# Optimization experiments

Hardware: AMD Instinct MI355X
Metric: run time of the kernel (lower is better)

The kernel has to match this reference:

```python
import jax, jax.numpy as jnp
import numpy as np

N_PATIENT = 50000
N_GENE = 20000
N_EDGE = 640000
P_DIM, G_DIM, H, OUT = 64, 32, 128, 8


def setup_inputs() -> dict:
    key = jax.random.key(0)
    ks = jax.random.split(key, 20)
    s = 0.02
    return {
        "x_patient": jax.random.normal(ks[0], (N_PATIENT, P_DIM), jnp.float32),
        "x_gene": jax.random.normal(ks[1], (N_GENE, G_DIM), jnp.float32),
        "edge_index": jax.random.randint(ks[2], (2, N_EDGE), 0, N_GENE, jnp.int32),
        # patient MLP
        "W_p1": jax.random.normal(ks[3], (P_DIM, H), jnp.float32) * s,
        "b_p1": jnp.zeros((H,), jnp.float32),
        "W_p2": jax.random.normal(ks[4], (H, H), jnp.float32) * s,
        "b_p2": jnp.zeros((H,), jnp.float32),
        # gene MLP
        "W_g1": jax.random.normal(ks[5], (G_DIM, H), jnp.float32) * s,
        "b_g1": jnp.zeros((H,), jnp.float32),
        "W_g2": jax.random.normal(ks[6], (H, H), jnp.float32) * s,
        "b_g2": jnp.zeros((H,), jnp.float32),
        # SAGEConv 1: lin_l acts on aggregated src, lin_r (root) on dst
        "W1_l": jax.random.normal(ks[7], (H, H), jnp.float32) * s,
        "b1_l": jnp.zeros((H,), jnp.float32),
        "W1_r": jax.random.normal(ks[8], (H, H), jnp.float32) * s,
        # SAGEConv 2
        "W2_l": jax.random.normal(ks[9], (H, H), jnp.float32) * s,
        "b2_l": jnp.zeros((H,), jnp.float32),
        "W2_r": jax.random.normal(ks[10], (H, H), jnp.float32) * s,
        # final fc
        "W_fc": jax.random.normal(ks[11], (H, OUT), jnp.float32) * s,
        "b_fc": jnp.zeros((OUT,), jnp.float32),
    }


def reference(x_patient, x_gene, edge_index,
              W_p1, b_p1, W_p2, b_p2,
              W_g1, b_g1, W_g2, b_g2,
              W1_l, b1_l, W1_r,
              W2_l, b2_l, W2_r,
              W_fc, b_fc):
    # node-type MLPs
    p = jax.nn.relu(x_patient @ W_p1 + b_p1) @ W_p2 + b_p2   # [N_P, H]
    g = jax.nn.relu(x_gene @ W_g1 + b_g1) @ W_g2 + b_g2       # [N_G, H]

    src, dst = edge_index[0], edge_index[1]
    # gene_x is unchanged between layers, so the sum-aggregate is identical
    # for both SAGEConv layers: compute the gather + segment-sum once.
    agg = jax.ops.segment_sum(g[src], dst, num_segments=x_patient.shape[0])  # [N_P, H]

    # SAGEConv(aggr='sum'): out = lin_l(agg) + lin_r(x_dst), bias in lin_l
    p = jax.nn.relu(agg @ W1_l + b1_l + p @ W1_r)
    p = jax.nn.relu(agg @ W2_l + b2_l + p @ W2_r)
    return p @ W_fc + b_fc  # [N_P, OUT]
```

## Files before the change

### kernel.cpp

```cpp
#include <hip/hip_runtime.h>

#define NP 50000
#define NG 20000
#define NE 640000
#define PD 64
#define GD 32
#define HD 128
#define OD 8
#define CAP 96
#define FILLB 125
#define EPB 5120

using f32x4 = __attribute__((ext_vector_type(4))) float;
using s16x8 = __attribute__((ext_vector_type(8))) short;

__device__ __forceinline__ unsigned short f2bf(float f) {
    union { float f; unsigned u; } v; v.f = f;
    const unsigned r = v.u + 0x7FFFu + ((v.u >> 16) & 1u);
    return (unsigned short)(r >> 16);
}
__device__ __forceinline__ float bfpair_lo(unsigned v) {
    union { unsigned u; float f; } x; x.u = v << 16; return x.f;
}
__device__ __forceinline__ float bfpair_hi(unsigned v) {
    union { unsigned u; float f; } x; x.u = v & 0xFFFF0000u; return x.f;
}

#define TOT_SWZ 112640

__global__ __launch_bounds__(256) void swz_kernel(
    const float* __restrict__ Wp1, const float* __restrict__ Wp2,
    const float* __restrict__ W1l, const float* __restrict__ W1r,
    const float* __restrict__ W2l, const float* __restrict__ W2r,
    const float* __restrict__ Wfc,
    const float* __restrict__ Wg1, const float* __restrict__ Wg2,
    unsigned short* __restrict__ wswz)
{
    const int u = blockIdx.x * 256 + threadIdx.x;
    if (u < TOT_SWZ) {
        const float* src; int K, Nr, doff;
        if      (u <   8192) { src = Wp1; K =  64; Nr = HD; doff = 0; }
        else if (u <  24576) { src = Wp2; K = 128; Nr = HD; doff = 8192; }
        else if (u <  40960) { src = W1l; K = 128; Nr = HD; doff = 24576; }
        else if (u <  57344) { src = W1r; K = 128; Nr = HD; doff = 40960; }
        else if (u <  73728) { src = W2l; K = 128; Nr = HD; doff = 57344; }
        else if (u <  90112) { src = W2r; K = 128; Nr = HD; doff = 73728; }
        else if (u <  92160) { src = Wfc; K = 128; Nr = OD; doff = 90112; }
        else if (u <  96256) { src = Wg1; K =  32; Nr = HD; doff = 92160; }
        else                 { src = Wg2; K = 128; Nr = HD; doff = 96256; }
        const int e  = u - doff;
        const int j  = e & 7;
        const int ln = (e >> 3) & 63;
        const int f  = e >> 9;
        const int KC = K >> 5;
        const int c  = f % KC;
        const int n0 = f / KC;
        const int k  = c * 32 + (ln >> 4) * 8 + j;
        const int n  = n0 * 16 + (ln & 15);
        wswz[u] = f2bf((n < Nr) ? src[k * Nr + n] : 0.f);
    }
}

#define GENE_TILES 313

__global__ __launch_bounds__(256) void genefill_kernel(
    const float* __restrict__ xg,
    const unsigned short* __restrict__ wswz,
    const float* __restrict__ bg1, const float* __restrict__ bg2,
    unsigned short* __restrict__ g,
    const int* __restrict__ ei, int* __restrict__ hist)
{
    __shared__ __align__(16) char smem[NG * 4];
    if (blockIdx.x >= GENE_TILES) {
        int* cnt = (int*)smem;
        const int tid = threadIdx.x;
#pragma unroll
        for (int k = 0; k < 20; ++k) {
            const int idx = k * 256 + tid;
            if (idx < NG / 4) ((int4*)cnt)[idx] = (int4){0, 0, 0, 0};
        }
        __syncthreads();
        const int base = (blockIdx.x - GENE_TILES) * EPB;
#pragma unroll
        for (int it = 0; it < 5; ++it) {
            const int e0 = base + it * 1024 + tid;
            const int d0 = ei[NE + e0];
            const int d1 = ei[NE + e0 + 256];
            const int d2 = ei[NE + e0 + 512];
            const int d3 = ei[NE + e0 + 768];
            atomicAdd(&cnt[d0], 1);
            atomicAdd(&cnt[d1], 1);
            atomicAdd(&cnt[d2], 1);
            atomicAdd(&cnt[d3], 1);
        }
        __syncthreads();
        int* Hb = hist + (blockIdx.x - GENE_TILES) * NG;
#pragma unroll
        for (int k = 0; k < 20; ++k) {
            const int idx = k * 256 + tid;
            if (idx < NG / 4) ((int4*)Hb)[idx] = ((int4*)cnt)[idx];
        }
        return;
    }
    const unsigned short* wg1 = wswz + 92160;
    const unsigned short* wg2 = wswz + 96256;

    const int lane = threadIdx.x & 63;
    const int wid  = threadIdx.x >> 6;
    const int quad = lane >> 4;
    const int l16  = lane & 15;
    const int row0 = blockIdx.x * 64 + wid * 16;
    const int arow = min(row0 + l16, NG - 1);
    unsigned short* X = (unsigned short*)smem + wid * 16 * 136;
    const f32x4 Z = {0.f, 0.f, 0.f, 0.f};

    s16x8 a;
    {
        const float* xr = xg + (size_t)arow * GD + quad * 8;
        const f32x4 u0 = *(const f32x4*)xr;
        const f32x4 u1 = *(const f32x4*)(xr + 4);
#pragma unroll
        for (int j = 0; j < 4; ++j) {
            a[j]     = (short)f2bf(u0[j]);
            a[4 + j] = (short)f2bf(u1[j]);
        }
    }
    f32x4 C[8];
#pragma unroll
    for (int n = 0; n < 8; ++n) {
        const s16x8 b = *(const s16x8*)&wg1[(n * 64 + lane) * 8];
        C[n] = __builtin_amdgcn_mfma_f32_16x16x32_bf16(a, b, Z, 0, 0, 0);
    }
#pragma unroll
    for (int n = 0; n < 8; ++n) {
        const float bias = bg1[n * 16 + l16];
#pragma unroll
        for (int r = 0; r < 4; ++r)
            X[(quad * 4 + r) * 136 + n * 16 + l16] = f2bf(fmaxf(C[n][r] + bias, 0.f));
    }
    __syncthreads();
    s16x8 pa[4];
#pragma unroll
    for (int c = 0; c < 4; ++c) pa[c] = *(const s16x8*)&X[l16 * 136 + c * 32 + quad * 8];
#pragma unroll
    for (int n = 0; n < 8; ++n) {
        C[n] = Z;
#pragma unroll
        for (int c = 0; c < 4; ++c) {
            const s16x8 b = *(const s16x8*)&wg2[((n * 4 + c) * 64 + lane) * 8];
            C[n] = __builtin_amdgcn_mfma_f32_16x16x32_bf16(pa[c], b, C[n], 0, 0, 0);
        }
    }
#pragma unroll
    for (int n = 0; n < 8; ++n) {
        const float bias = bg2[n * 16 + l16];
#pragma unroll
        for (int r = 0; r < 4; ++r) {
            const int row = row0 + quad * 4 + r;
            if (row < NG) g[(size_t)row * HD + n * 16 + l16] = f2bf(C[n][r] + bias);
        }
    }
}

__global__ __launch_bounds__(256) void scan_kernel(
    int* __restrict__ hist, int* __restrict__ cursor)
{
    const int d = blockIdx.x * 256 + threadIdx.x;
    if (d >= NG) return;
    int run = 0;
#pragma unroll 5
    for (int b = 0; b < FILLB; ++b) {
        const int t = hist[b * NG + d];
        hist[b * NG + d] = run;
        run += t;
    }
    cursor[d] = run;
}

__global__ __launch_bounds__(256) void place_kernel(
    const int* __restrict__ ei, const int* __restrict__ hist,
    unsigned short* __restrict__ pad)
{
    __shared__ __align__(16) int cnt[NG];
    const int tid = threadIdx.x;
    const int* Hb = hist + blockIdx.x * NG;
#pragma unroll
    for (int k = 0; k < 20; ++k) {
        const int idx = k * 256 + tid;
        if (idx < NG / 4) ((int4*)cnt)[idx] = ((const int4*)Hb)[idx];
    }
    __syncthreads();
    const int base = blockIdx.x * EPB;
#pragma unroll
    for (int it = 0; it < 5; ++it) {
        const int e0 = base + it * 1024 + tid;
        const int s0 = ei[e0];       const int d0 = ei[NE + e0];
        const int s1 = ei[e0 + 256]; const int d1 = ei[NE + e0 + 256];
        const int s2 = ei[e0 + 512]; const int d2 = ei[NE + e0 + 512];
        const int s3 = ei[e0 + 768]; const int d3 = ei[NE + e0 + 768];
        { const int p = atomicAdd(&cnt[d0], 1); if (p < CAP) pad[d0 * CAP + p] = (unsigned short)s0; }
        { const int p = atomicAdd(&cnt[d1], 1); if (p < CAP) pad[d1 * CAP + p] = (unsigned short)s1; }
        { const int p = atomicAdd(&cnt[d2], 1); if (p < CAP) pad[d2 * CAP + p] = (unsigned short)s2; }
        { const int p = atomicAdd(&cnt[d3], 1); if (p < CAP) pad[d3 * CAP + p] = (unsigned short)s3; }
    }
}

__global__ __launch_bounds__(256) void agg_kernel(
    const int* __restrict__ cursor, const unsigned short* __restrict__ pad,
    const unsigned short* __restrict__ g, unsigned short* __restrict__ aggb)
{
    const int row  = blockIdx.x * 4 + (threadIdx.x >> 6);
    const int lane = threadIdx.x & 63;
    const int grp  = lane >> 4;
    const int sub  = lane & 15;

    float acc[8] = {0.f, 0.f, 0.f, 0.f, 0.f, 0.f, 0.f, 0.f};
    const int cnt = min(cursor[row], CAP);
    const size_t rb = (size_t)row * CAP;
    for (int i = grp * 4; i < cnt; i += 16) {
        const ushort4 q = *(const ushort4*)&pad[rb + i];
        int r0 = q.x, r1 = q.y, r2 = q.z, r3 = q.w;
        const bool v1 = (i + 1) < cnt, v2 = (i + 2) < cnt, v3 = (i + 3) < cnt;
        r1 = v1 ? r1 : r0;  r2 = v2 ? r2 : r0;  r3 = v3 ? r3 : r0;
        const float s1 = v1 ? 1.f : 0.f, s2 = v2 ? 1.f : 0.f, s3 = v3 ? 1.f : 0.f;
        const s16x8 g0 = *(const s16x8*)&g[(size_t)r0 * HD + sub * 8];
        const s16x8 g1 = *(const s16x8*)&g[(size_t)r1 * HD + sub * 8];
        const s16x8 g2 = *(const s16x8*)&g[(size_t)r2 * HD + sub * 8];
        const s16x8 g3 = *(const s16x8*)&g[(size_t)r3 * HD + sub * 8];
        const unsigned* d0 = (const unsigned*)&g0;
        const unsigned* d1 = (const unsigned*)&g1;
        const unsigned* d2 = (const unsigned*)&g2;
        const unsigned* d3 = (const unsigned*)&g3;
#pragma unroll
        for (int k = 0; k < 4; ++k) {
            acc[2 * k]     += bfpair_lo(d0[k]);
            acc[2 * k + 1] += bfpair_hi(d0[k]);
            acc[2 * k]     = fmaf(bfpair_lo(d1[k]), s1, acc[2 * k]);
            acc[2 * k + 1] = fmaf(bfpair_hi(d1[k]), s1, acc[2 * k + 1]);
            acc[2 * k]     = fmaf(bfpair_lo(d2[k]), s2, acc[2 * k]);
            acc[2 * k + 1] = fmaf(bfpair_hi(d2[k]), s2, acc[2 * k + 1]);
            acc[2 * k]     = fmaf(bfpair_lo(d3[k]), s3, acc[2 * k]);
            acc[2 * k + 1] = fmaf(bfpair_hi(d3[k]), s3, acc[2 * k + 1]);
        }
    }
#pragma unroll
    for (int k = 0; k < 8; ++k) {
        acc[k] += __shfl_xor(acc[k], 16);
        acc[k] += __shfl_xor(acc[k], 32);
    }
    if (lane < 16) {
        unsigned o[4];
#pragma unroll
        for (int k = 0; k < 4; ++k)
            o[k] = (unsigned)f2bf(acc[2 * k]) | ((unsigned)f2bf(acc[2 * k + 1]) << 16);
        *(int4*)&aggb[(size_t)row * HD + lane * 8] = *(int4*)o;
    }
}

__global__ __launch_bounds__(256) void patient_kernel(
    const float* __restrict__ xp, const unsigned short* __restrict__ aggb,
    const unsigned short* __restrict__ wswz,
    const float* __restrict__ bp1, const float* __restrict__ bp2,
    const float* __restrict__ b1l, const float* __restrict__ b2l,
    const float* __restrict__ bfc,
    float* __restrict__ out)
{
    const unsigned short* wp1 = wswz + 0;
    const unsigned short* wp2 = wswz + 8192;
    const unsigned short* w1l = wswz + 24576;
    const unsigned short* w1r = wswz + 40960;
    const unsigned short* w2l = wswz + 57344;
    const unsigned short* w2r = wswz + 73728;
    const unsigned short* wfc = wswz + 90112;

    __shared__ __align__(16) unsigned short XA[128 * 136];
    __shared__ __align__(16) unsigned short AG[128 * 136];

    const int tid  = threadIdx.x;
    const int lane = tid & 63;
    const int wid  = tid >> 6;
    const int quad = lane >> 4;
    const int l16  = lane & 15;
    const int brow = blockIdx.x * 128;
    const bool hasAgg = (brow < NG);
    const int nA = wid * 2, nB = wid * 2 + 1;
    const f32x4 Z = {0.f, 0.f, 0.f, 0.f};

#pragma unroll
    for (int s = 0; s < 8; ++s) {
        const int slot = s * 256 + tid;
        const int r  = slot >> 4;
        const int cv = slot & 15;
        const f32x4 u = *(const f32x4*)&xp[(size_t)min(brow + r, NP - 1) * PD + cv * 4];
        unsigned short o[4];
#pragma unroll
        for (int j = 0; j < 4; ++j) o[j] = f2bf(u[j]);
        *(ushort4*)&XA[r * 136 + cv * 4] = *(ushort4*)o;
    }
    if (hasAgg) {
#pragma unroll
        for (int s = 0; s < 8; ++s) {
            const int slot = s * 256 + tid;
            const int r  = slot >> 4;
            const int cv = slot & 15;
            const int gr = brow + r;
            s16x8 v = {0, 0, 0, 0, 0, 0, 0, 0};
            if (gr < NG) v = *(const s16x8*)&aggb[(size_t)gr * HD + cv * 8];
            *(s16x8*)&AG[r * 136 + cv * 8] = v;
        }
    }
    __syncthreads();

    f32x4 acc[8][2];

#pragma unroll
    for (int rt = 0; rt < 8; ++rt) { acc[rt][0] = Z; acc[rt][1] = Z; }
#pragma unroll
    for (int c = 0; c < 2; ++c) {
        const s16x8 b0 = *(const s16x8*)&wp1[((nA * 2 + c) * 64 + lane) * 8];
        const s16x8 b1 = *(const s16x8*)&wp1[((nB * 2 + c) * 64 + lane) * 8];
#pragma unroll
        for (int rt = 0; rt < 8; ++rt) {
            const s16x8 a = *(const s16x8*)&XA[(rt * 16 + l16) * 136 + c * 32 + quad * 8];
            acc[rt][0] = __builtin_amdgcn_mfma_f32_16x16x32_bf16(a, b0, acc[rt][0], 0, 0, 0);
            acc[rt][1] = __builtin_amdgcn_mfma_f32_16x16x32_bf16(a, b1, acc[rt][1], 0, 0, 0);
        }
    }
    __syncthreads();
#pragma unroll
    for (int t = 0; t < 2; ++t) {
        const int n = wid * 2 + t;
        const float bias = bp1[n * 16 + l16];
#pragma unroll
        for (int rt = 0; rt < 8; ++rt)
#pragma unroll
            for (int r = 0; r < 4; ++r)
                XA[(rt * 16 + quad * 4 + r) * 136 + n * 16 + l16] =
                    f2bf(fmaxf(acc[rt][t][r] + bias, 0.f));
    }
    __syncthreads();

#pragma unroll
    for (int rt = 0; rt < 8; ++rt) { acc[rt][0] = Z; acc[rt][1] = Z; }
#pragma unroll
    for (int c = 0; c < 4; ++c) {
        const s16x8 b0 = *(const s16x8*)&wp2[((nA * 4 + c) * 64 + lane) * 8];
        const s16x8 b1 = *(const s16x8*)&wp2[((nB * 4 + c) * 64 + lane) * 8];
#pragma unroll
        for (int rt = 0; rt < 8; ++rt) {
            const s16x8 a = *(const s16x8*)&XA[(rt * 16 + l16) * 136 + c * 32 + quad * 8];
            acc[rt][0] = __builtin_amdgcn_mfma_f32_16x16x32_bf16(a, b0, acc[rt][0], 0, 0, 0);
            acc[rt][1] = __builtin_amdgcn_mfma_f32_16x16x32_bf16(a, b1, acc[rt][1], 0, 0, 0);
        }
    }
    __syncthreads();
#pragma unroll
    for (int t = 0; t < 2; ++t) {
        const int n = wid * 2 + t;
        const float bias = bp2[n * 16 + l16];
#pragma unroll
        for (int rt = 0; rt < 8; ++rt)
#pragma unroll
            for (int r = 0; r < 4; ++r)
                XA[(rt * 16 + quad * 4 + r) * 136 + n * 16 + l16] =
                    f2bf(acc[rt][t][r] + bias);
    }
    __syncthreads();

#pragma unroll
    for (int rt = 0; rt < 8; ++rt) { acc[rt][0] = Z; acc[rt][1] = Z; }
    if (hasAgg) {
#pragma unroll
        for (int c = 0; c < 4; ++c) {
            const s16x8 br0 = *(const s16x8*)&w1r[((nA * 4 + c) * 64 + lane) * 8];
            const s16x8 br1 = *(const s16x8*)&w1r[((nB * 4 + c) * 64 + lane) * 8];
            const s16x8 bl0 = *(const s16x8*)&w1l[((nA * 4 + c) * 64 + lane) * 8];
            const s16x8 bl1 = *(const s16x8*)&w1l[((nB * 4 + c) * 64 + lane) * 8];
#pragma unroll
            for (int rt = 0; rt < 8; ++rt) {
                const s16x8 ap = *(const s16x8*)&XA[(rt * 16 + l16) * 136 + c * 32 + quad * 8];
                const s16x8 ag = *(const s16x8*)&AG[(rt * 16 + l16) * 136 + c * 32 + quad * 8];
                acc[rt][0] = __builtin_amdgcn_mfma_f32_16x16x32_bf16(ap, br0, acc[rt][0], 0, 0, 0);
                acc[rt][0] = __builtin_amdgcn_mfma_f32_16x16x32_bf16(ag, bl0, acc[rt][0], 0, 0, 0);
                acc[rt][1] = __builtin_amdgcn_mfma_f32_16x16x32_bf16(ap, br1, acc[rt][1], 0, 0, 0);
                acc[rt][1] = __builtin_amdgcn_mfma_f32_16x16x32_bf16(ag, bl1, acc[rt][1], 0, 0, 0);
            }
        }
    } else {
#pragma unroll
        for (int c = 0; c < 4; ++c) {
            const s16x8 br0 = *(const s16x8*)&w1r[((nA * 4 + c) * 64 + lane) * 8];
            const s16x8 br1 = *(const s16x8*)&w1r[((nB * 4 + c) * 64 + lane) * 8];
#pragma unroll
            for (int rt = 0; rt < 8; ++rt) {
                const s16x8 ap = *(const s16x8*)&XA[(rt * 16 + l16) * 136 + c * 32 + quad * 8];
                acc[rt][0] = __builtin_amdgcn_mfma_f32_16x16x32_bf16(ap, br0, acc[rt][0], 0, 0, 0);
                acc[rt][1] = __builtin_amdgcn_mfma_f32_16x16x32_bf16(ap, br1, acc[rt][1], 0, 0, 0);
            }
        }
    }
    __syncthreads();
#pragma unroll
    for (int t = 0; t < 2; ++t) {
        const int n = wid * 2 + t;
        const float bias = b1l[n * 16 + l16];
#pragma unroll
        for (int rt = 0; rt < 8; ++rt)
#pragma unroll
            for (int r = 0; r < 4; ++r)
                XA[(rt * 16 + quad * 4 + r) * 136 + n * 16 + l16] =
                    f2bf(fmaxf(acc[rt][t][r] + bias, 0.f));
    }
    __syncthreads();

#pragma unroll
    for (int rt = 0; rt < 8; ++rt) { acc[rt][0] = Z; acc[rt][1] = Z; }
    if (hasAgg) {
#pragma unroll
        for (int c = 0; c < 4; ++c) {
            const s16x8 br0 = *(const s16x8*)&w2r[((nA * 4 + c) * 64 + lane) * 8];
            const s16x8 br1 = *(const s16x8*)&w2r[((nB * 4 + c) * 64 + lane) * 8];
            const s16x8 bl0 = *(const s16x8*)&w2l[((nA * 4 + c) * 64 + lane) * 8];
            const s16x8 bl1 = *(const s16x8*)&w2l[((nB * 4 + c) * 64 + lane) * 8];
#pragma unroll
            for (int rt = 0; rt < 8; ++rt) {
                const s16x8 ap = *(const s16x8*)&XA[(rt * 16 + l16) * 136 + c * 32 + quad * 8];
                const s16x8 ag = *(const s16x8*)&AG[(rt * 16 + l16) * 136 + c * 32 + quad * 8];
                acc[rt][0] = __builtin_amdgcn_mfma_f32_16x16x32_bf16(ap, br0, acc[rt][0], 0, 0, 0);
                acc[rt][0] = __builtin_amdgcn_mfma_f32_16x16x32_bf16(ag, bl0, acc[rt][0], 0, 0, 0);
                acc[rt][1] = __builtin_amdgcn_mfma_f32_16x16x32_bf16(ap, br1, acc[rt][1], 0, 0, 0);
                acc[rt][1] = __builtin_amdgcn_mfma_f32_16x16x32_bf16(ag, bl1, acc[rt][1], 0, 0, 0);
            }
        }
    } else {
#pragma unroll
        for (int c = 0; c < 4; ++c) {
            const s16x8 br0 = *(const s16x8*)&w2r[((nA * 4 + c) * 64 + lane) * 8];
            const s16x8 br1 = *(const s16x8*)&w2r[((nB * 4 + c) * 64 + lane) * 8];
#pragma unroll
            for (int rt = 0; rt < 8; ++rt) {
                const s16x8 ap = *(const s16x8*)&XA[(rt * 16 + l16) * 136 + c * 32 + quad * 8];
                acc[rt][0] = __builtin_amdgcn_mfma_f32_16x16x32_bf16(ap, br0, acc[rt][0], 0, 0, 0);
                acc[rt][1] = __builtin_amdgcn_mfma_f32_16x16x32_bf16(ap, br1, acc[rt][1], 0, 0, 0);
            }
        }
    }
    __syncthreads();
#pragma unroll
    for (int t = 0; t < 2; ++t) {
        const int n = wid * 2 + t;
        const float bias = b2l[n * 16 + l16];
#pragma unroll
        for (int rt = 0; rt < 8; ++rt)
#pragma unroll
            for (int r = 0; r < 4; ++r)
                XA[(rt * 16 + quad * 4 + r) * 136 + n * 16 + l16] =
                    f2bf(fmaxf(acc[rt][t][r] + bias, 0.f));
    }
    __syncthreads();

    {
        f32x4 co[2] = {Z, Z};
#pragma unroll
        for (int c = 0; c < 4; ++c) {
            const s16x8 b = *(const s16x8*)&wfc[(c * 64 + lane) * 8];
#pragma unroll
            for (int j = 0; j < 2; ++j) {
                const int rt = wid * 2 + j;
                const s16x8 a = *(const s16x8*)&XA[(rt * 16 + l16) * 136 + c * 32 + quad * 8];
                co[j] = __builtin_amdgcn_mfma_f32_16x16x32_bf16(a, b, co[j], 0, 0, 0);
            }
        }
        if (l16 < OD) {
            const float bias = bfc[l16];
#pragma unroll
            for (int j = 0; j < 2; ++j)
#pragma unroll
                for (int r = 0; r < 4; ++r) {
                    const int row = brow + (wid * 2 + j) * 16 + quad * 4 + r;
                    if (row < NP) out[(size_t)row * OD + l16] = co[j][r] + bias;
                }
        }
    }
}

extern "C" void kernel_launch(void* const* d_in, const int* in_sizes, int n_in,
                              void* d_out, int out_size, void* d_ws, size_t ws_size,
                              hipStream_t stream)
{
    const float* xp  = (const float*)d_in[0];
    const float* xg  = (const float*)d_in[1];
    const int*   ei  = (const int*)d_in[2];
    const float* Wp1 = (const float*)d_in[3];
    const float* bp1 = (const float*)d_in[4];
    const float* Wp2 = (const float*)d_in[5];
    const float* bp2 = (const float*)d_in[6];
    const float* Wg1 = (const float*)d_in[7];
    const float* bg1 = (const float*)d_in[8];
    const float* Wg2 = (const float*)d_in[9];
    const float* bg2 = (const float*)d_in[10];
    const float* W1l = (const float*)d_in[11];
    const float* b1l = (const float*)d_in[12];
    const float* W1r = (const float*)d_in[13];
    const float* W2l = (const float*)d_in[14];
    const float* b2l = (const float*)d_in[15];
    const float* W2r = (const float*)d_in[16];
    const float* Wfc = (const float*)d_in[17];
    const float* bfc = (const float*)d_in[18];
    float* out = (float*)d_out;

    char* ws = (char*)d_ws;
    unsigned short* g_b   = (unsigned short*)(ws + 0);
    unsigned short* wswz  = (unsigned short*)(ws + 5120000);
    int*            cursor= (int*)(ws + 5345280);
    int*            hist  = (int*)(ws + 5425280);
    unsigned short* pad   = (unsigned short*)(ws + 15425280);
    unsigned short* agg_b = (unsigned short*)(ws + 19265280);

    swz_kernel<<<(TOT_SWZ + 255) / 256, 256, 0, stream>>>(
        Wp1, Wp2, W1l, W1r, W2l, W2r, Wfc, Wg1, Wg2, wswz);

    genefill_kernel<<<GENE_TILES + FILLB, 256, 0, stream>>>(
        xg, wswz, bg1, bg2, g_b, ei, hist);

    scan_kernel<<<(NG + 255) / 256, 256, 0, stream>>>(hist, cursor);

    place_kernel<<<FILLB, 256, 0, stream>>>(ei, hist, pad);

    agg_kernel<<<NG / 4, 256, 0, stream>>>(cursor, pad, g_b, agg_b);

    patient_kernel<<<(NP + 127) / 128, 256, 0, stream>>>(
        xp, agg_b, wswz, bp1, bp2, b1l, b2l, bfc, out);
}
```

Before: 163.1 us.

## Replace histogram/scan edge bucketing with global atomics and restructure kernel schedule

Drops the per-block histogram, scan and shared-memory place kernels. Edges are now bucketed directly with global atomicAdd on a cursor array that the swizzle kernel zeroes, and this placement runs in the same launch as the gene MLP. The aggregation blocks are merged into the patient-MLP launch so the gather overlaps with the patient rows that have no aggregate. Patient rows below NG write their MLP output to a buffer, and a separate SAGE kernel finishes them. The gains are fewer launches and less hist traffic; the costs are contention on global atomics and an extra round trip through memory for p.

Result: slower. 194.1 us (+19.0%).

```diff
diff --git a/kernel.cpp b/kernel.cpp
--- a/kernel.cpp
+++ b/kernel.cpp
@@ -8,8 +8,10 @@
 #define HD 128
 #define OD 8
 #define CAP 96
-#define FILLB 125
-#define EPB 5120
+#define PLACEB 625
+#define GENE_TILES 313
+#define PATB 391
+#define SAGEB 157
 
 using f32x4 = __attribute__((ext_vector_type(4))) float;
 using s16x8 = __attribute__((ext_vector_type(8))) short;
@@ -34,7 +36,7 @@
     const float* __restrict__ W2l, const float* __restrict__ W2r,
     const float* __restrict__ Wfc,
     const float* __restrict__ Wg1, const float* __restrict__ Wg2,
-    unsigned short* __restrict__ wswz)
+    unsigned short* __restrict__ wswz, int* __restrict__ cursor)
 {
     const int u = blockIdx.x * 256 + threadIdx.x;
     if (u < TOT_SWZ) {
@@ -58,48 +60,32 @@
         const int k  = c * 32 + (ln >> 4) * 8 + j;
         const int n  = n0 * 16 + (ln & 15);
         wswz[u] = f2bf((n < Nr) ? src[k * Nr + n] : 0.f);
-    }
-}
-
-#define GENE_TILES 313
-
-__global__ __launch_bounds__(256) void genefill_kernel(
+    } else {
+        const int d = u - TOT_SWZ;
+        if (d < NG) cursor[d] = 0;
+    }
+}
+
+__global__ __launch_bounds__(256) void geneplace_kernel(
     const float* __restrict__ xg,
     const unsigned short* __restrict__ wswz,
     const float* __restrict__ bg1, const float* __restrict__ bg2,
     unsigned short* __restrict__ g,
-    const int* __restrict__ ei, int* __restrict__ hist)
+    const int* __restrict__ ei,
+    int* __restrict__ cursor, unsigned short* __restrict__ pad)
 {
-    __shared__ __align__(16) char smem[NG * 4];
+    __shared__ __align__(16) unsigned short smem[4 * 16 * 136];
     if (blockIdx.x >= GENE_TILES) {
-        int* cnt = (int*)smem;
-        const int tid = threadIdx.x;
-#pragma unroll
-        for (int k = 0; k < 20; ++k) {
-            const int idx = k * 256 + tid;
-            if (idx < NG / 4) ((int4*)cnt)[idx] = (int4){0, 0, 0, 0};
-        }
-        __syncthreads();
-        const int base = (blockIdx.x - GENE_TILES) * EPB;
-#pragma unroll
-        for (int it = 0; it < 5; ++it) {
-            const int e0 = base + it * 1024 + tid;
-            const int d0 = ei[NE + e0];
-            const int d1 = ei[NE + e0 + 256];
-            const int d2 = ei[NE + e0 + 512];
-            const int d3 = ei[NE + e0 + 768];
-            atomicAdd(&cnt[d0], 1);
-            atomicAdd(&cnt[d1], 1);
-            atomicAdd(&cnt[d2], 1);
-            atomicAdd(&cnt[d3], 1);
-        }
-        __syncthreads();
-        int* Hb = hist + (blockIdx.x - GENE_TILES) * NG;
-#pragma unroll
-        for (int k = 0; k < 20; ++k) {
-            const int idx = k * 256 + tid;
-            if (idx < NG / 4) ((int4*)Hb)[idx] = ((int4*)cnt)[idx];
-        }
+        const int base = (blockIdx.x - GENE_TILES) * 1024;
+        const int e0 = base + threadIdx.x;
+        const int s0 = ei[e0];       const int d0 = ei[NE + e0];
+        const int s1 = ei[e0 + 256]; const int d1 = ei[NE + e0 + 256];
+        const int s2 = ei[e0 + 512]; const int d2 = ei[NE + e0 + 512];
+        const int s3 = ei[e0 + 768]; const int d3 = ei[NE + e0 + 768];
+        { const int p = atomicAdd(&cursor[d0], 1); if (p < CAP) pad[d0 * CAP + p] = (unsigned short)s0; }
+        { const int p = atomicAdd(&cursor[d1], 1); if (p < CAP) pad[d1 * CAP + p] = (unsigned short)s1; }
+        { const int p = atomicAdd(&cursor[d2], 1); if (p < CAP) pad[d2 * CAP + p] = (unsigned short)s2; }
+        { const int p = atomicAdd(&cursor[d3], 1); if (p < CAP) pad[d3 * CAP + p] = (unsigned short)s3; }
         return;
     }
     const unsigned short* wg1 = wswz + 92160;
@@ -111,7 +97,7 @@
     const int l16  = lane & 15;
     const int row0 = blockIdx.x * 64 + wid * 16;
     const int arow = min(row0 + l16, NG - 1);
-    unsigned short* X = (unsigned short*)smem + wid * 16 * 136;
+    unsigned short* X = smem + wid * 16 * 136;
     const f32x4 Z = {0.f, 0.f, 0.f, 0.f};
 
     s16x8 a;
@@ -162,119 +148,74 @@
     }
 }
 
-__global__ __launch_bounds__(256) void scan_kernel(
-    int* __restrict__ hist, int* __restrict__ cursor)
-{
-    const int d = blockIdx.x * 256 + threadIdx.x;
-    if (d >= NG) return;
-    int run = 0;
-#pragma unroll 5
-    for (int b = 0; b < FILLB; ++b) {
-        const int t = hist[b * NG + d];
-        hist[b * NG + d] = run;
-        run += t;
-    }
-    cursor[d] = run;
-}
-
-__global__ __launch_bounds__(256) void place_kernel(
-    const int* __restrict__ ei, const int* __restrict__ hist,
-    unsigned short* __restrict__ pad)
-{
-    __shared__ __align__(16) int cnt[NG];
-    const int tid = threadIdx.x;
-    const int* Hb = hist + blockIdx.x * NG;
-#pragma unroll
-    for (int k = 0; k < 20; ++k) {
-        const int idx = k * 256 + tid;
-        if (idx < NG / 4) ((int4*)cnt)[idx] = ((const int4*)Hb)[idx];
-    }
-    __syncthreads();
-    const int base = blockIdx.x * EPB;
-#pragma unroll
-    for (int it = 0; it < 5; ++it) {
-        const int e0 = base + it * 1024 + tid;
-        const int s0 = ei[e0];       const int d0 = ei[NE + e0];
-        const int s1 = ei[e0 + 256]; const int d1 = ei[NE + e0 + 256];
-        const int s2 = ei[e0 + 512]; const int d2 = ei[NE + e0 + 512];
-        const int s3 = ei[e0 + 768]; const int d3 = ei[NE + e0 + 768];
-        { const int p = atomicAdd(&cnt[d0], 1); if (p < CAP) pad[d0 * CAP + p] = (unsigned short)s0; }
-        { const int p = atomicAdd(&cnt[d1], 1); if (p < CAP) pad[d1 * CAP + p] = (unsigned short)s1; }
-        { const int p = atomicAdd(&cnt[d2], 1); if (p < CAP) pad[d2 * CAP + p] = (unsigned short)s2; }
-        { const int p = atomicAdd(&cnt[d3], 1); if (p < CAP) pad[d3 * CAP + p] = (unsigned short)s3; }
-    }
-}
-
-__global__ __launch_bounds__(256) void agg_kernel(
+__global__ __launch_bounds__(256) void patient3_kernel(
+    const float* __restrict__ xp,
+    const unsigned short* __restrict__ g,
     const int* __restrict__ cursor, const unsigned short* __restrict__ pad,
-    const unsigned short* __restrict__ g, unsigned short* __restrict__ aggb)
-{
-    const int row  = blockIdx.x * 4 + (threadIdx.x >> 6);
-    const int lane = threadIdx.x & 63;
-    const int grp  = lane >> 4;
-    const int sub  = lane & 15;
-
-    float acc[8] = {0.f, 0.f, 0.f, 0.f, 0.f, 0.f, 0.f, 0.f};
-    const int cnt = min(cursor[row], CAP);
-    const size_t rb = (size_t)row * CAP;
-    for (int i = grp * 4; i < cnt; i += 16) {
-        const ushort4 q = *(const ushort4*)&pad[rb + i];
-        int r0 = q.x, r1 = q.y, r2 = q.z, r3 = q.w;
-        const bool v1 = (i + 1) < cnt, v2 = (i + 2) < cnt, v3 = (i + 3) < cnt;
-        r1 = v1 ? r1 : r0;  r2 = v2 ? r2 : r0;  r3 = v3 ? r3 : r0;
-        const float s1 = v1 ? 1.f : 0.f, s2 = v2 ? 1.f : 0.f, s3 = v3 ? 1.f : 0.f;
-        const s16x8 g0 = *(const s16x8*)&g[(size_t)r0 * HD + sub * 8];
-        const s16x8 g1 = *(const s16x8*)&g[(size_t)r1 * HD + sub * 8];
-        const s16x8 g2 = *(const s16x8*)&g[(size_t)r2 * HD + sub * 8];
-        const s16x8 g3 = *(const s16x8*)&g[(size_t)r3 * HD + sub * 8];
-        const unsigned* d0 = (const unsigned*)&g0;
-        const unsigned* d1 = (const unsigned*)&g1;
-        const unsigned* d2 = (const unsigned*)&g2;
-        const unsigned* d3 = (const unsigned*)&g3;
-#pragma unroll
-        for (int k = 0; k < 4; ++k) {
-            acc[2 * k]     += bfpair_lo(d0[k]);
-            acc[2 * k + 1] += bfpair_hi(d0[k]);
-            acc[2 * k]     = fmaf(bfpair_lo(d1[k]), s1, acc[2 * k]);
-            acc[2 * k + 1] = fmaf(bfpair_hi(d1[k]), s1, acc[2 * k + 1]);
-            acc[2 * k]     = fmaf(bfpair_lo(d2[k]), s2, acc[2 * k]);
-            acc[2 * k + 1] = fmaf(bfpair_hi(d2[k]), s2, acc[2 * k + 1]);
-            acc[2 * k]     = fmaf(bfpair_lo(d3[k]), s3, acc[2 * k]);
-            acc[2 * k + 1] = fmaf(bfpair_hi(d3[k]), s3, acc[2 * k + 1]);
-        }
-    }
-#pragma unroll
-    for (int k = 0; k < 8; ++k) {
-        acc[k] += __shfl_xor(acc[k], 16);
-        acc[k] += __shfl_xor(acc[k], 32);
-    }
-    if (lane < 16) {
-        unsigned o[4];
-#pragma unroll
-        for (int k = 0; k < 4; ++k)
-            o[k] = (unsigned)f2bf(acc[2 * k]) | ((unsigned)f2bf(acc[2 * k + 1]) << 16);
-        *(int4*)&aggb[(size_t)row * HD + lane * 8] = *(int4*)o;
-    }
-}
-
-__global__ __launch_bounds__(256) void patient_kernel(
-    const float* __restrict__ xp, const unsigned short* __restrict__ aggb,
     const unsigned short* __restrict__ wswz,
     const float* __restrict__ bp1, const float* __restrict__ bp2,
     const float* __restrict__ b1l, const float* __restrict__ b2l,
     const float* __restrict__ bfc,
+    unsigned short* __restrict__ p_b, unsigned short* __restrict__ aggb,
     float* __restrict__ out)
 {
+    __shared__ __align__(16) unsigned short XA[128 * 136];
+
+    if (blockIdx.x >= PATB) {
+        const int row  = (blockIdx.x - PATB) * 4 + (threadIdx.x >> 6);
+        const int lane = threadIdx.x & 63;
+        const int grp  = lane >> 4;
+        const int sub  = lane & 15;
+
+        float acc[8] = {0.f, 0.f, 0.f, 0.f, 0.f, 0.f, 0.f, 0.f};
+        const int cnt = min(cursor[row], CAP);
+        const size_t rb = (size_t)row * CAP;
+        for (int i = grp * 4; i < cnt; i += 16) {
+            const ushort4 q = *(const ushort4*)&pad[rb + i];
+            int r0 = q.x, r1 = q.y, r2 = q.z, r3 = q.w;
+            const bool v1 = (i + 1) < cnt, v2 = (i + 2) < cnt, v3 = (i + 3) < cnt;
+            r1 = v1 ? r1 : r0;  r2 = v2 ? r2 : r0;  r3 = v3 ? r3 : r0;
+            const float s1 = v1 ? 1.f : 0.f, s2 = v2 ? 1.f : 0.f, s3 = v3 ? 1.f : 0.f;
+            const s16x8 g0 = *(const s16x8*)&g[(size_t)r0 * HD + sub * 8];
+            const s16x8 g1 = *(const s16x8*)&g[(size_t)r1 * HD + sub * 8];
+            const s16x8 g2 = *(const s16x8*)&g[(size_t)r2 * HD + sub * 8];
+            const s16x8 g3 = *(const s16x8*)&g[(size_t)r3 * HD + sub * 8];
+            const unsigned* d0 = (const unsigned*)&g0;
+            const unsigned* d1 = (const unsigned*)&g1;
+            const unsigned* d2 = (const unsigned*)&g2;
+            const unsigned* d3 = (const unsigned*)&g3;
+#pragma unroll
+            for (int k = 0; k < 4; ++k) {
+                acc[2 * k]     += bfpair_lo(d0[k]);
+                acc[2 * k + 1] += bfpair_hi(d0[k]);
+                acc[2 * k]     = fmaf(bfpair_lo(d1[k]), s1, acc[2 * k]);
+                acc[2 * k + 1] = fmaf(bfpair_hi(d1[k]), s1, acc[2 * k + 1]);
+                acc[2 * k]     = fmaf(bfpair_lo(d2[k]), s2, acc[2 * k]);
+                acc[2 * k + 1] = fmaf(bfpair_hi(d2[k]), s2, acc[2 * k + 1]);
+                acc[2 * k]     = fmaf(bfpair_lo(d3[k]), s3, acc[2 * k]);
+                acc[2 * k + 1] = fmaf(bfpair_hi(d3[k]), s3, acc[2 * k + 1]);
+            }
+        }
+#pragma unroll
+        for (int k = 0; k < 8; ++k) {
+            acc[k] += __shfl_xor(acc[k], 16);
+            acc[k] += __shfl_xor(acc[k], 32);
+        }
+        if (lane < 16) {
+            unsigned o[4];
+#pragma unroll
+            for (int k = 0; k < 4; ++k)
+                o[k] = (unsigned)f2bf(acc[2 * k]) | ((unsigned)f2bf(acc[2 * k + 1]) << 16);
+            *(int4*)&aggb[(size_t)row * HD + lane * 8] = *(int4*)o;
+        }
+        return;
+    }
+
     const unsigned short* wp1 = wswz + 0;
     const unsigned short* wp2 = wswz + 8192;
-    const unsigned short* w1l = wswz + 24576;
     const unsigned short* w1r = wswz + 40960;
-    const unsigned short* w2l = wswz + 57344;
     const unsigned short* w2r = wswz + 73728;
     const unsigned short* wfc = wswz + 90112;
-
-    __shared__ __align__(16) unsigned short XA[128 * 136];
-    __shared__ __align__(16) unsigned short AG[128 * 136];
 
     const int tid  = threadIdx.x;
     const int lane = tid & 63;
@@ -282,7 +223,6 @@
     const int quad = lane >> 4;
     const int l16  = lane & 15;
     const int brow = blockIdx.x * 128;
-    const bool hasAgg = (brow < NG);
     const int nA = wid * 2, nB = wid * 2 + 1;
     const f32x4 Z = {0.f, 0.f, 0.f, 0.f};
 
@@ -297,18 +237,6 @@
         for (int j = 0; j < 4; ++j) o[j] = f2bf(u[j]);
         *(ushort4*)&XA[r * 136 + cv * 4] = *(ushort4*)o;
     }
-    if (hasAgg) {
-#pragma unroll
-        for (int s = 0; s < 8; ++s) {
-            const int slot = s * 256 + tid;
-            const int r  = slot >> 4;
-            const int cv = slot & 15;
-            const int gr = brow + r;
-            s16x8 v = {0, 0, 0, 0, 0, 0, 0, 0};
-            if (gr < NG) v = *(const s16x8*)&aggb[(size_t)gr * HD + cv * 8];
-            *(s16x8*)&AG[r * 136 + cv * 8] = v;
-        }
-    }
     __syncthreads();
 
     f32x4 acc[8][2];
@@ -353,6 +281,22 @@
             acc[rt][1] = __builtin_amdgcn_mfma_f32_16x16x32_bf16(a, b1, acc[rt][1], 0, 0, 0);
         }
     }
+
+    if (brow < NG) {
+#pragma unroll
+        for (int t = 0; t < 2; ++t) {
+            const int n = wid * 2 + t;
+            const float bias = bp2[n * 16 + l16];
+#pragma unroll
+            for (int rt = 0; rt < 8; ++rt)
+#pragma unroll
+                for (int r = 0; r < 4; ++r)
+                    p_b[(size_t)(brow + rt * 16 + quad * 4 + r) * HD + n * 16 + l16] =
+                        f2bf(acc[rt][t][r] + bias);
+        }
+        return;
+    }
+
     __syncthreads();
 #pragma unroll
     for (int t = 0; t < 2; ++t) {
@@ -369,34 +313,15 @@
 
 #pragma unroll
     for (int rt = 0; rt < 8; ++rt) { acc[rt][0] = Z; acc[rt][1] = Z; }
-    if (hasAgg) {
-#pragma unroll
-        for (int c = 0; c < 4; ++c) {
-            const s16x8 br0 = *(const s16x8*)&w1r[((nA * 4 + c) * 64 + lane) * 8];
-            const s16x8 br1 = *(const s16x8*)&w1r[((nB * 4 + c) * 64 + lane) * 8];
-            const s16x8 bl0 = *(const s16x8*)&w1l[((nA * 4 + c) * 64 + lane) * 8];
-            const s16x8 bl1 = *(const s16x8*)&w1l[((nB * 4 + c) * 64 + lane) * 8];
-#pragma unroll
-            for (int rt = 0; rt < 8; ++rt) {
-                const s16x8 ap = *(const s16x8*)&XA[(rt * 16 + l16) * 136 + c * 32 + quad * 8];
-                const s16x8 ag = *(const s16x8*)&AG[(rt * 16 + l16) * 136 + c * 32 + quad * 8];
-                acc[rt][0] = __builtin_amdgcn_mfma_f32_16x16x32_bf16(ap, br0, acc[rt][0], 0, 0, 0);
-                acc[rt][0] = __builtin_amdgcn_mfma_f32_16x16x32_bf16(ag, bl0, acc[rt][0], 0, 0, 0);
-                acc[rt][1] = __builtin_amdgcn_mfma_f32_16x16x32_bf16(ap, br1, acc[rt][1], 0, 0, 0);
-                acc[rt][1] = __builtin_amdgcn_mfma_f32_16x16x32_bf16(ag, bl1, acc[rt][1], 0, 0, 0);
-            }
-        }
-    } else {
-#pragma unroll
-        for (int c = 0; c < 4; ++c) {
-            const s16x8 br0 = *(const s16x8*)&w1r[((nA * 4 + c) * 64 + lane) * 8];
-            const s16x8 br1 = *(const s16x8*)&w1r[((nB * 4 + c) * 64 + lane) * 8];
-#pragma unroll
-            for (int rt = 0; rt < 8; ++rt) {
-                const s16x8 ap = *(const s16x8*)&XA[(rt * 16 + l16) * 136 + c * 32 + quad * 8];
-                acc[rt][0] = __builtin_amdgcn_mfma_f32_16x16x32_bf16(ap, br0, acc[rt][0], 0, 0, 0);
-                acc[rt][1] = __builtin_amdgcn_mfma_f32_16x16x32_bf16(ap, br1, acc[rt][1], 0, 0, 0);
-            }
+#pragma unroll
+    for (int c = 0; c < 4; ++c) {
+        const s16x8 b0 = *(const s16x8*)&w1r[((nA * 4 + c) * 64 + lane) * 8];
+        const s16x8 b1 = *(const s16x8*)&w1r[((nB * 4 + c) * 64 + lane) * 8];
+#pragma unroll
+        for (int rt = 0; rt < 8; ++rt) {
+            const s16x8 a = *(const s16x8*)&XA[(rt * 16 + l16) * 136 + c * 32 + quad * 8];
+            acc[rt][0] = __builtin_amdgcn_mfma_f32_16x16x32_bf16(a, b0, acc[rt][0], 0, 0, 0);
+            acc[rt][1] = __builtin_amdgcn_mfma_f32_16x16x32_bf16(a, b1, acc[rt][1], 0, 0, 0);
         }
     }
     __syncthreads();
@@ -415,34 +340,144 @@
 
 #pragma unroll
     for (int rt = 0; rt < 8; ++rt) { acc[rt][0] = Z; acc[rt][1] = Z; }
-    if (hasAgg) {
+#pragma unroll
+    for (int c = 0; c < 4; ++c) {
+        const s16x8 b0 = *(const s16x8*)&w2r[((nA * 4 + c) * 64 + lane) * 8];
+        const s16x8 b1 = *(const s16x8*)&w2r[((nB * 4 + c) * 64 + lane) * 8];
+#pragma unroll
+        for (int rt = 0; rt < 8; ++rt) {
+            const s16x8 a = *(const s16x8*)&XA[(rt * 16 + l16) * 136 + c * 32 + quad * 8];
+            acc[rt][0] = __builtin_amdgcn_mfma_f32_16x16x32_bf16(a, b0, acc[rt][0], 0, 0, 0);
+            acc[rt][1] = __builtin_amdgcn_mfma_f32_16x16x32_bf16(a, b1, acc[rt][1], 0, 0, 0);
+        }
+    }
+    __syncthreads();
+#pragma unroll
+    for (int t = 0; t < 2; ++t) {
+        const int n = wid * 2 + t;
+        const float bias = b2l[n * 16 + l16];
+#pragma unroll
+        for (int rt = 0; rt < 8; ++rt)
+#pragma unroll
+            for (int r = 0; r < 4; ++r)
+                XA[(rt * 16 + quad * 4 + r) * 136 + n * 16 + l16] =
+                    f2bf(fmaxf(acc[rt][t][r] + bias, 0.f));
+    }
+    __syncthreads();
+
+    {
+        f32x4 co[2] = {Z, Z};
 #pragma unroll
         for (int c = 0; c < 4; ++c) {
-            const s16x8 br0 = *(const s16x8*)&w2r[((nA * 4 + c) * 64 + lane) * 8];
-            const s16x8 br1 = *(const s16x8*)&w2r[((nB * 4 + c) * 64 + lane) * 8];
-            const s16x8 bl0 = *(const s16x8*)&w2l[((nA * 4 + c) * 64 + lane) * 8];
-            const s16x8 bl1 = *(const s16x8*)&w2l[((nB * 4 + c) * 64 + lane) * 8];
-#pragma unroll
-            for (int rt = 0; rt < 8; ++rt) {
-                const s16x8 ap = *(const s16x8*)&XA[(rt * 16 + l16) * 136 + c * 32 + quad * 8];
-                const s16x8 ag = *(const s16x8*)&AG[(rt * 16 + l16) * 136 + c * 32 + quad * 8];
-                acc[rt][0] = __builtin_amdgcn_mfma_f32_16x16x32_bf16(ap, br0, acc[rt][0], 0, 0, 0);
-                acc[rt][0] = __builtin_amdgcn_mfma_f32_16x16x32_bf16(ag, bl0, acc[rt][0], 0, 0, 0);
-                acc[rt][1] = __builtin_amdgcn_mfma_f32_16x16x32_bf16(ap, br1, acc[rt][1], 0, 0, 0);
-                acc[rt][1] = __builtin_amdgcn_mfma_f32_16x16x32_bf16(ag, bl1, acc[rt][1], 0, 0, 0);
+            const s16x8 b = *(const s16x8*)&wfc[(c * 64 + lane) * 8];
+#pragma unroll
+            for (int j = 0; j < 2; ++j) {
+                const int rt = wid * 2 + j;
+                const s16x8 a = *(const s16x8*)&XA[(rt * 16 + l16) * 136 + c * 32 + quad * 8];
+                co[j] = __builtin_amdgcn_mfma_f32_16x16x32_bf16(a, b, co[j], 0, 0, 0);
             }
         }
-    } else {
-#pragma unroll
-        for (int c = 0; c < 4; ++c) {
-            const s16x8 br0 = *(const s16x8*)&w2r[((nA * 4 + c) * 64 + lane) * 8];
-            const s16x8 br1 = *(const s16x8*)&w2r[((nB * 4 + c) * 64 + lane) * 8];
-#pragma unroll
-            for (int rt = 0; rt < 8; ++rt) {
-                const s16x8 ap = *(const s16x8*)&XA[(rt * 16 + l16) * 136 + c * 32 + quad * 8];
-                acc[rt][0] = __builtin_amdgcn_mfma_f32_16x16x32_bf16(ap, br0, acc[rt][0], 0, 0, 0);
-                acc[rt][1] = __builtin_amdgcn_mfma_f32_16x16x32_bf16(ap, br1, acc[rt][1], 0, 0, 0);
-            }
+        if (l16 < OD) {
+            const float bias = bfc[l16];
+#pragma unroll
+            for (int j = 0; j < 2; ++j)
+#pragma unroll
+                for (int r = 0; r < 4; ++r) {
+                    const int row = brow + (wid * 2 + j) * 16 + quad * 4 + r;
+                    if (row < NP) out[(size_t)row * OD + l16] = co[j][r] + bias;
+                }
+        }
+    }
+}
+
+__global__ __launch_bounds__(256) void sage_kernel(
+    const unsigned short* __restrict__ p_b, const unsigned short* __restrict__ aggb,
+    const unsigned short* __restrict__ wswz,
+    const float* __restrict__ b1l, const float* __restrict__ b2l,
+    const float* __restrict__ bfc,
+    float* __restrict__ out)
+{
+    const unsigned short* w1l = wswz + 24576;
+    const unsigned short* w1r = wswz + 40960;
+    const unsigned short* w2l = wswz + 57344;
+    const unsigned short* w2r = wswz + 73728;
+    const unsigned short* wfc = wswz + 90112;
+
+    __shared__ __align__(16) unsigned short XA[128 * 136];
+    __shared__ __align__(16) unsigned short AG[128 * 136];
+
+    const int tid  = threadIdx.x;
+    const int lane = tid & 63;
+    const int wid  = tid >> 6;
+    const int quad = lane >> 4;
+    const int l16  = lane & 15;
+    const int brow = blockIdx.x * 128;
+    const int nA = wid * 2, nB = wid * 2 + 1;
+    const f32x4 Z = {0.f, 0.f, 0.f, 0.f};
+
+#pragma unroll
+    for (int s = 0; s < 8; ++s) {
+        const int slot = s * 256 + tid;
+        const int r  = slot >> 4;
+        const int cv = slot & 15;
+        const int gr = brow + r;
+        *(s16x8*)&XA[r * 136 + cv * 8] = *(const s16x8*)&p_b[(size_t)gr * HD + cv * 8];
+        s16x8 v = {0, 0, 0, 0, 0, 0, 0, 0};
+        if (gr < NG) v = *(const s16x8*)&aggb[(size_t)gr * HD + cv * 8];
+        *(s16x8*)&AG[r * 136 + cv * 8] = v;
+    }
+    __syncthreads();
+
+    f32x4 acc[8][2];
+
+#pragma unroll
+    for (int rt = 0; rt < 8; ++rt) { acc[rt][0] = Z; acc[rt][1] = Z; }
+#pragma unroll
+    for (int c = 0; c < 4; ++c) {
+        const s16x8 br0 = *(const s16x8*)&w1r[((nA * 4 + c) * 64 + lane) * 8];
+        const s16x8 br1 = *(const s16x8*)&w1r[((nB * 4 + c) * 64 + lane) * 8];
+        const s16x8 bl0 = *(const s16x8*)&w1l[((nA * 4 + c) * 64 + lane) * 8];
+        const s16x8 bl1 = *(const s16x8*)&w1l[((nB * 4 + c) * 64 + lane) * 8];
+#pragma unroll
+        for (int rt = 0; rt < 8; ++rt) {
+            const s16x8 ap = *(const s16x8*)&XA[(rt * 16 + l16) * 136 + c * 32 + quad * 8];
+            const s16x8 ag = *(const s16x8*)&AG[(rt * 16 + l16) * 136 + c * 32 + quad * 8];
+            acc[rt][0] = __builtin_amdgcn_mfma_f32_16x16x32_bf16(ap, br0, acc[rt][0], 0, 0, 0);
+            acc[rt][0] = __builtin_amdgcn_mfma_f32_16x16x32_bf16(ag, bl0, acc[rt][0], 0, 0, 0);
+            acc[rt][1] = __builtin_amdgcn_mfma_f32_16x16x32_bf16(ap, br1, acc[rt][1], 0, 0, 0);
+            acc[rt][1] = __builtin_amdgcn_mfma_f32_16x16x32_bf16(ag, bl1, acc[rt][1], 0, 0, 0);
+        }
+    }
+    __syncthreads();
+#pragma unroll
+    for (int t = 0; t < 2; ++t) {
+        const int n = wid * 2 + t;
+        const float bias = b1l[n * 16 + l16];
+#pragma unroll
+        for (int rt = 0; rt < 8; ++rt)
+#pragma unroll
+            for (int r = 0; r < 4; ++r)
+                XA[(rt * 16 + quad * 4 + r) * 136 + n * 16 + l16] =
+                    f2bf(fmaxf(acc[rt][t][r] + bias, 0.f));
+    }
+    __syncthreads();
+
+#pragma unroll
+    for (int rt = 0; rt < 8; ++rt) { acc[rt][0] = Z; acc[rt][1] = Z; }
+#pragma unroll
+    for (int c = 0; c < 4; ++c) {
+        const s16x8 br0 = *(const s16x8*)&w2r[((nA * 4 + c) * 64 + lane) * 8];
+        const s16x8 br1 = *(const s16x8*)&w2r[((nB * 4 + c) * 64 + lane) * 8];
+        const s16x8 bl0 = *(const s16x8*)&w2l[((nA * 4 + c) * 64 + lane) * 8];
+        const s16x8 bl1 = *(const s16x8*)&w2l[((nB * 4 + c) * 64 + lane) * 8];
+#pragma unroll
+        for (int rt = 0; rt < 8; ++rt) {
+            const s16x8 ap = *(const s16x8*)&XA[(rt * 16 + l16) * 136 + c * 32 + quad * 8];
+            const s16x8 ag = *(const s16x8*)&AG[(rt * 16 + l16) * 136 + c * 32 + quad * 8];
+            acc[rt][0] = __builtin_amdgcn_mfma_f32_16x16x32_bf16(ap, br0, acc[rt][0], 0, 0, 0);
+            acc[rt][0] = __builtin_amdgcn_mfma_f32_16x16x32_bf16(ag, bl0, acc[rt][0], 0, 0, 0);
+            acc[rt][1] = __builtin_amdgcn_mfma_f32_16x16x32_bf16(ap, br1, acc[rt][1], 0, 0, 0);
+            acc[rt][1] = __builtin_amdgcn_mfma_f32_16x16x32_bf16(ag, bl1, acc[rt][1], 0, 0, 0);
         }
     }
     __syncthreads();
@@ -513,22 +548,19 @@
     unsigned short* g_b   = (unsigned short*)(ws + 0);
     unsigned short* wswz  = (unsigned short*)(ws + 5120000);
     int*            cursor= (int*)(ws + 5345280);
-    int*            hist  = (int*)(ws + 5425280);
-    unsigned short* pad   = (unsigned short*)(ws + 15425280);
-    unsigned short* agg_b = (unsigned short*)(ws + 19265280);
-
-    swz_kernel<<<(TOT_SWZ + 255) / 256, 256, 0, stream>>>(
-        Wp1, Wp2, W1l, W1r, W2l, W2r, Wfc, Wg1, Wg2, wswz);
-
-    genefill_kernel<<<GENE_TILES + FILLB, 256, 0, stream>>>(
-        xg, wswz, bg1, bg2, g_b, ei, hist);
-
-    scan_kernel<<<(NG + 255) / 256, 256, 0, stream>>>(hist, cursor);
-
-    place_kernel<<<FILLB, 256, 0, stream>>>(ei, hist, pad);
-
-    agg_kernel<<<NG / 4, 256, 0, stream>>>(cursor, pad, g_b, agg_b);
-
-    patient_kernel<<<(NP + 127) / 128, 256, 0, stream>>>(
-        xp, agg_b, wswz, bp1, bp2, b1l, b2l, bfc, out);
-}
+    unsigned short* pad   = (unsigned short*)(ws + 5425280);
+    unsigned short* p_b   = (unsigned short*)(ws + 9265280);
+    unsigned short* agg_b = (unsigned short*)(ws + 14409856);
+
+    swz_kernel<<<(TOT_SWZ + NG + 255) / 256, 256, 0, stream>>>(
+        Wp1, Wp2, W1l, W1r, W2l, W2r, Wfc, Wg1, Wg2, wswz, cursor);
+
+    geneplace_kernel<<<GENE_TILES + PLACEB, 256, 0, stream>>>(
+        xg, wswz, bg1, bg2, g_b, ei, cursor, pad);
+
+    patient3_kernel<<<PATB + NG / 4, 256, 0, stream>>>(
+        xp, g_b, cursor, pad, wswz, bp1, bp2, b1l, b2l, bfc, p_b, agg_b, out);
+
+    sage_kernel<<<SAGEB, 256, 0, stream>>>(
+        p_b, agg_b, wswz, b1l, b2l, bfc, out);
+}
```
